# Optimization experiments

Hardware: AMD Instinct MI355X
Metric: run time of the kernel (lower is better)

The kernel has to match this reference:

```python
import jax, jax.numpy as jnp
import numpy as np


def _graph_conv(x, W, b, src, dst, norm_src, norm_dst, n_nodes):
    # DGL GraphConv, norm='both': out = D_in^{-1/2} * A * D_out^{-1/2} * x * W + b
    h = x * norm_src[:, None]                      # [N, d] scale by src out-degree norm
    m = h[src]                                     # [E, d] gather (irregular access)
    agg = jax.ops.segment_sum(m, dst, num_segments=n_nodes)  # [N, d] scatter-add
    agg = agg * norm_dst[:, None]
    return agg @ W + b


def setup_inputs() -> dict:
    key = jax.random.key(0)
    ks = jax.random.split(key, 6)
    N, E, IN, HID = 50000, 800000, 64, 128
    in_feat = jax.random.normal(ks[0], (N, IN), dtype=jnp.float32)
    W1 = jax.random.normal(ks[1], (IN, HID), dtype=jnp.float32) * (1.0 / np.sqrt(IN))
    b1 = jnp.zeros((HID,), dtype=jnp.float32)
    W2 = jax.random.normal(ks[2], (HID, IN), dtype=jnp.float32) * (1.0 / np.sqrt(HID))
    b2 = jnp.zeros((IN,), dtype=jnp.float32)
    src = jax.random.randint(ks[3], (E,), 0, N, dtype=jnp.int32)
    dst = jax.random.randint(ks[4], (E,), 0, N, dtype=jnp.int32)
    return {"in_feat": in_feat, "W1": W1, "b1": b1, "W2": W2, "b2": b2,
            "src": src, "dst": dst, "n_nodes": N}


def reference(in_feat, W1, b1, W2, b2, src, dst, n_nodes):
    ones = jnp.ones(src.shape, dtype=in_feat.dtype)
    deg_out = jax.ops.segment_sum(ones, src, num_segments=n_nodes)
    deg_in = jax.ops.segment_sum(ones, dst, num_segments=n_nodes)
    # DGL clamps degrees to min 1 (allow_zero_in_degree=True just skips the check)
    norm_src = jnp.clip(deg_out, 1.0, None) ** -0.5
    norm_dst = jnp.clip(deg_in, 1.0, None) ** -0.5
    h = _graph_conv(in_feat, W1, b1, src, dst, norm_src, norm_dst, n_nodes)
    h = jax.nn.relu(h)
    h = _graph_conv(h, W2, b2, src, dst, norm_src, norm_dst, n_nodes)
    return h
```

## Files before the change

kernel.cpp:

```cpp
#include <hip/hip_runtime.h>

#define IN_F 64
#define HID_F 128
#define CAP 64
#define CHUNK 4096
#define CAPB 4096
#define MAXB 512

typedef unsigned short u16;
typedef unsigned int u32;
typedef _Float16 f16;
typedef __attribute__((ext_vector_type(4))) _Float16 f16x4;
typedef __attribute__((ext_vector_type(8))) _Float16 f16x8;
typedef __attribute__((ext_vector_type(4))) float f32x4;

__global__ __launch_bounds__(256)
void partition_kernel(const int* __restrict__ src, const int* __restrict__ dst,
                      int* __restrict__ gcurD, int* __restrict__ gcurS,
                      u32* __restrict__ bufD, u16* __restrict__ bufS,
                      int E, int NBUCK) {
    __shared__ int histD[MAXB], histS[MAXB], baseD[MAXB], baseS[MAXB];
    const int t  = threadIdx.x;
    const int e0 = blockIdx.x * CHUNK;
    const int n  = min(CHUNK, E - e0);

    for (int b = t; b < NBUCK; b += 256) { histD[b] = 0; histS[b] = 0; }
    __syncthreads();
    for (int i = t; i < n; i += 256) {
        atomicAdd(&histD[dst[e0 + i] >> 7], 1);
        atomicAdd(&histS[src[e0 + i] >> 7], 1);
    }
    __syncthreads();
    for (int b = t; b < NBUCK; b += 256) {
        baseD[b] = atomicAdd(&gcurD[b], histD[b]);
        baseS[b] = atomicAdd(&gcurS[b], histS[b]);
        histD[b] = 0;
        histS[b] = 0;
    }
    __syncthreads();
    for (int i = t; i < n; i += 256) {
        int d  = dst[e0 + i];
        int s  = src[e0 + i];
        int bD = d >> 7, bS = s >> 7;
        int p  = baseD[bD] + atomicAdd(&histD[bD], 1);
        if (p < CAPB) bufD[(size_t)bD * CAPB + p] = (u32)d | ((u32)s << 16);
        int p2 = baseS[bS] + atomicAdd(&histS[bS], 1);
        if (p2 < CAPB) bufS[(size_t)bS * CAPB + p2] = (u16)s;
    }
}

__global__ __launch_bounds__(256)
void bucket_pass2_kernel(const u32* __restrict__ bufD, const int* __restrict__ gcurD,
                         const u16* __restrict__ bufS, const int* __restrict__ gcurS,
                         u16* __restrict__ slots, int* __restrict__ deg_in,
                         int* __restrict__ deg_out, int N, int NBUCK) {
    __shared__ int lcur[128];
    const int t = threadIdx.x;
    if (t < 128) lcur[t] = 0;
    __syncthreads();
    if (blockIdx.x < NBUCK) {
        const int b = blockIdx.x;
        const int cnt = min(gcurD[b], CAPB);
        const u32* p = bufD + (size_t)b * CAPB;
        for (int i = t; i < cnt; i += 256) {
            u32 v = p[i];
            int d = (int)(v & 0xFFFFu);
            int s = (int)(v >> 16);
            int pos = atomicAdd(&lcur[d & 127], 1);
            if (pos < CAP) slots[(size_t)d * CAP + pos] = (u16)s;
        }
        __syncthreads();
        int node = b * 128 + t;
        if (t < 128 && node < N) deg_in[node] = lcur[t];
    } else {
        const int b = blockIdx.x - NBUCK;
        const int cnt = min(gcurS[b], CAPB);
        const u16* p = bufS + (size_t)b * CAPB;
        for (int i = t; i < cnt; i += 256)
            atomicAdd(&lcur[p[i] & 127], 1);
        __syncthreads();
        int node = b * 128 + t;
        if (t < 128 && node < N) deg_out[node] = lcur[t];
    }
}

__global__ void prep_w_kernel(const float* __restrict__ W1, const float* __restrict__ W2,
                              f16* __restrict__ W1t, f16* __restrict__ W2t) {
    int t = blockIdx.x * blockDim.x + threadIdx.x;
    if (t < IN_F * HID_F) {
        int n = t / IN_F, k = t % IN_F;
        W1t[t] = (f16)W1[k * HID_F + n];
    } else if (t < 2 * IN_F * HID_F) {
        int i = t - IN_F * HID_F;
        int n = i / HID_F, k = i % HID_F;
        W2t[i] = (f16)W2[k * IN_F + n];
    }
}

__global__ void norm_prescale_kernel(const int* __restrict__ dego, const int* __restrict__ degi,
                                     const float* __restrict__ x,
                                     float* __restrict__ norm_src, float* __restrict__ norm_dst,
                                     f16x4* __restrict__ y, int N) {
    int t = blockIdx.x * blockDim.x + threadIdx.x;
    if (t < N * 16) {
        int r = t >> 4;
        int c = t & 15;
        float ns = rsqrtf((float)max(dego[r], 1));
        float4 v = ((const float4*)x)[t];
        f16x4 h;
        h.x = (f16)(v.x * ns); h.y = (f16)(v.y * ns);
        h.z = (f16)(v.z * ns); h.w = (f16)(v.w * ns);
        y[t] = h;
        if (c == 0) {
            norm_src[r] = ns;
            norm_dst[r] = rsqrtf((float)max(degi[r], 1));
        }
    }
}

template <bool DST_EPI>
__global__ void gather_agg_kernel(const f16x4* __restrict__ x, const u16* __restrict__ slots,
                                  const int* __restrict__ deg_in, const float* __restrict__ sd,
                                  const float* __restrict__ bias,
                                  void* __restrict__ outv, int N) {
    int t = blockIdx.x * blockDim.x + threadIdx.x;
    int node = t >> 4;
    int c = t & 15;
    if (node >= N) return;
    int deg = min(deg_in[node], CAP);
    const u16* srow = slots + (size_t)node * CAP;
    float4 acc = make_float4(0.f, 0.f, 0.f, 0.f);

    int i = 0;
    for (; i + 8 <= deg; i += 8) {
        int s[8];
#pragma unroll
        for (int j = 0; j < 8; ++j) s[j] = (int)srow[i + j];
        f16x4 v[8];
#pragma unroll
        for (int j = 0; j < 8; ++j) v[j] = x[(size_t)s[j] * 16 + c];
#pragma unroll
        for (int j = 0; j < 8; ++j) {
            acc.x += (float)v[j].x; acc.y += (float)v[j].y;
            acc.z += (float)v[j].z; acc.w += (float)v[j].w;
        }
    }
    for (; i < deg; ++i) {
        f16x4 v = x[(size_t)srow[i] * 16 + c];
        acc.x += (float)v.x; acc.y += (float)v.y;
        acc.z += (float)v.z; acc.w += (float)v.w;
    }
    if (DST_EPI) {
        float d = sd[node];
        float4 bb = ((const float4*)bias)[c];
        acc.x = acc.x * d + bb.x;
        acc.y = acc.y * d + bb.y;
        acc.z = acc.z * d + bb.z;
        acc.w = acc.w * d + bb.w;
        ((float4*)outv)[t] = acc;
    } else {
        f16x4 h;
        h.x = (f16)acc.x; h.y = (f16)acc.y; h.z = (f16)acc.z; h.w = (f16)acc.w;
        ((f16x4*)outv)[t] = h;
    }
}

template <int K, int NCOL, bool RELU, bool BIAS>
__global__ __launch_bounds__(256)
void gemm_mfma(const f16* __restrict__ A, const f16* __restrict__ Wt,
               const float* __restrict__ bias, const float* __restrict__ rowscale,
               f16* __restrict__ C, int M) {
    constexpr int KT = K / 32;
    constexpr int CT = NCOL / 16;
    const int wave = threadIdx.x >> 6;
    const int lane = threadIdx.x & 63;
    const int nl   = lane & 15;
    const int quad = lane >> 4;
    const int tile = blockIdx.x * 4 + wave;
    if (tile * 16 >= M) return;
    const int r0 = tile * 16;

    f16x8 b[CT][KT];
#pragma unroll
    for (int ct = 0; ct < CT; ++ct)
#pragma unroll
        for (int kf = 0; kf < KT; ++kf)
            b[ct][kf] = *(const f16x8*)(Wt + (ct * 16 + nl) * K + kf * 32 + quad * 8);

    f16x8 a[KT];
#pragma unroll
    for (int kf = 0; kf < KT; ++kf)
        a[kf] = *(const f16x8*)(A + (size_t)(r0 + nl) * K + kf * 32 + quad * 8);

    f32x4 acc[CT];
#pragma unroll
    for (int ct = 0; ct < CT; ++ct) acc[ct] = (f32x4){0.f, 0.f, 0.f, 0.f};
#pragma unroll
    for (int ct = 0; ct < CT; ++ct)
#pragma unroll
        for (int kf = 0; kf < KT; ++kf)
            acc[ct] = __builtin_amdgcn_mfma_f32_16x16x32_f16(a[kf], b[ct][kf], acc[ct], 0, 0, 0);

    float rs[4];
#pragma unroll
    for (int reg = 0; reg < 4; ++reg) rs[reg] = rowscale[r0 + quad * 4 + reg];
#pragma unroll
    for (int ct = 0; ct < CT; ++ct) {
        float bb = BIAS ? bias[ct * 16 + nl] : 0.f;
#pragma unroll
        for (int reg = 0; reg < 4; ++reg) {
            float v = acc[ct][reg] * rs[reg] + bb;
            if (RELU) v = fmaxf(v, 0.f);
            C[(size_t)(r0 + quad * 4 + reg) * NCOL + ct * 16 + nl] = (f16)v;
        }
    }
}

extern "C" void kernel_launch(void* const* d_in, const int* in_sizes, int n_in,
                              void* d_out, int out_size, void* d_ws, size_t ws_size,
                              hipStream_t stream) {
    const float* in_feat = (const float*)d_in[0];
    const float* W1      = (const float*)d_in[1];
    const float* b1      = (const float*)d_in[2];
    const float* W2      = (const float*)d_in[3];
    const float* b2      = (const float*)d_in[4];
    const int*   src     = (const int*)d_in[5];
    const int*   dst     = (const int*)d_in[6];

    const int N = in_sizes[0] / IN_F;
    const int E = in_sizes[5];
    float* out = (float*)d_out;

    const int NBUCK = (N + 127) >> 7;

    int* deg_in  = (int*)d_ws;
    int* deg_out = deg_in + N;
    int* gcurD   = deg_out + N;
    int* gcurS   = gcurD + MAXB;
    u16* slots   = (u16*)(gcurS + MAXB);
    float* norm_src = (float*)(slots + (size_t)N * CAP);
    float* norm_dst = norm_src + N;
    f16* scaled_x = (f16*)(norm_dst + N);
    f16* agg1     = scaled_x + (size_t)N * IN_F;
    f16* h1       = agg1 + (size_t)N * IN_F;
    f16* g2       = h1 + (size_t)N * HID_F;
    f16* W1t      = g2 + (size_t)N * IN_F;
    f16* W2t      = W1t + IN_F * HID_F;
    u32* bufD     = (u32*)(W2t + IN_F * HID_F);
    u16* bufS     = (u16*)(bufD + (size_t)NBUCK * CAPB);

    hipMemsetAsync(gcurD, 0, sizeof(int) * 2 * MAXB, stream);
    prep_w_kernel<<<(2 * IN_F * HID_F + 255) / 256, 256, 0, stream>>>(W1, W2, W1t, W2t);
    partition_kernel<<<(E + CHUNK - 1) / CHUNK, 256, 0, stream>>>(
        src, dst, gcurD, gcurS, bufD, bufS, E, NBUCK);
    bucket_pass2_kernel<<<2 * NBUCK, 256, 0, stream>>>(
        bufD, gcurD, bufS, gcurS, slots, deg_in, deg_out, N, NBUCK);

    const int gthreads = N * 16;
    const int gblocks  = (gthreads + 255) / 256;
    const int mfma_blocks = ((N + 15) / 16 + 3) / 4;

    norm_prescale_kernel<<<gblocks, 256, 0, stream>>>(
        deg_out, deg_in, in_feat, norm_src, norm_dst, (f16x4*)scaled_x, N);

    gather_agg_kernel<false><<<gblocks, 256, 0, stream>>>(
        (const f16x4*)scaled_x, slots, deg_in, nullptr, nullptr, agg1, N);
    gemm_mfma<IN_F, HID_F, true, true><<<mfma_blocks, 256, 0, stream>>>(
        agg1, W1t, b1, norm_dst, h1, N);

    gemm_mfma<HID_F, IN_F, false, false><<<mfma_blocks, 256, 0, stream>>>(
        h1, W2t, nullptr, norm_src, g2, N);
    gather_agg_kernel<true><<<gblocks, 256, 0, stream>>>(
        (const f16x4*)g2, slots, deg_in, norm_dst, b2, out, N);
}
```

Before: 179.8 us.

## Fuse the two MFMA GEMMs through LDS and fold weight prep into partition

The two per-node GEMMs (agg1·W1 with ReLU, then h1·W2 with the source-norm scale) now run in one kernel. The hidden activations stay in per-wave shared memory instead of going through a global h1 buffer, which removes one kernel launch and a write and read of N×128 halves. Weight transposition moves into an extra block of the partition kernel, dropping another launch. The intra-wave handoff through LDS relies on s_waitcnt with no barrier, which assumes wave-synchronous execution, and W fragments are now loaded inside the MFMA loop rather than hoisted.

```diff
diff --git a/kernel.cpp b/kernel.cpp
--- a/kernel.cpp
+++ b/kernel.cpp
@@ -18,7 +18,22 @@
 void partition_kernel(const int* __restrict__ src, const int* __restrict__ dst,
                       int* __restrict__ gcurD, int* __restrict__ gcurS,
                       u32* __restrict__ bufD, u16* __restrict__ bufS,
+                      const float* __restrict__ W1, const float* __restrict__ W2,
+                      f16* __restrict__ W1t, f16* __restrict__ W2t,
                       int E, int NBUCK) {
+    if (blockIdx.x == gridDim.x - 1) {
+        for (int t = threadIdx.x; t < 2 * IN_F * HID_F; t += 256) {
+            if (t < IN_F * HID_F) {
+                int n = t / IN_F, k = t % IN_F;
+                W1t[t] = (f16)W1[k * HID_F + n];
+            } else {
+                int i = t - IN_F * HID_F;
+                int n = i / HID_F, k = i % HID_F;
+                W2t[i] = (f16)W2[k * IN_F + n];
+            }
+        }
+        return;
+    }
     __shared__ int histD[MAXB], histS[MAXB], baseD[MAXB], baseS[MAXB];
     const int t  = threadIdx.x;
     const int e0 = blockIdx.x * CHUNK;
@@ -81,19 +96,6 @@
         __syncthreads();
         int node = b * 128 + t;
         if (t < 128 && node < N) deg_out[node] = lcur[t];
-    }
-}
-
-__global__ void prep_w_kernel(const float* __restrict__ W1, const float* __restrict__ W2,
-                              f16* __restrict__ W1t, f16* __restrict__ W2t) {
-    int t = blockIdx.x * blockDim.x + threadIdx.x;
-    if (t < IN_F * HID_F) {
-        int n = t / IN_F, k = t % IN_F;
-        W1t[t] = (f16)W1[k * HID_F + n];
-    } else if (t < 2 * IN_F * HID_F) {
-        int i = t - IN_F * HID_F;
-        int n = i / HID_F, k = i % HID_F;
-        W2t[i] = (f16)W2[k * IN_F + n];
     }
 }
 
@@ -165,13 +167,13 @@
     }
 }
 
-template <int K, int NCOL, bool RELU, bool BIAS>
 __global__ __launch_bounds__(256)
-void gemm_mfma(const f16* __restrict__ A, const f16* __restrict__ Wt,
-               const float* __restrict__ bias, const float* __restrict__ rowscale,
-               f16* __restrict__ C, int M) {
-    constexpr int KT = K / 32;
-    constexpr int CT = NCOL / 16;
+void gemm_fused(const f16* __restrict__ agg1, const f16* __restrict__ W1t,
+                const float* __restrict__ b1, const float* __restrict__ nd,
+                const float* __restrict__ ns, const f16* __restrict__ W2t,
+                f16* __restrict__ g2, int M) {
+    constexpr int LDH = HID_F + 8;
+    __shared__ f16 h[4][16 * LDH];
     const int wave = threadIdx.x >> 6;
     const int lane = threadIdx.x & 63;
     const int nl   = lane & 15;
@@ -179,41 +181,63 @@
     const int tile = blockIdx.x * 4 + wave;
     if (tile * 16 >= M) return;
     const int r0 = tile * 16;
-
-    f16x8 b[CT][KT];
-#pragma unroll
-    for (int ct = 0; ct < CT; ++ct)
-#pragma unroll
-        for (int kf = 0; kf < KT; ++kf)
-            b[ct][kf] = *(const f16x8*)(Wt + (ct * 16 + nl) * K + kf * 32 + quad * 8);
-
-    f16x8 a[KT];
-#pragma unroll
-    for (int kf = 0; kf < KT; ++kf)
-        a[kf] = *(const f16x8*)(A + (size_t)(r0 + nl) * K + kf * 32 + quad * 8);
-
-    f32x4 acc[CT];
-#pragma unroll
-    for (int ct = 0; ct < CT; ++ct) acc[ct] = (f32x4){0.f, 0.f, 0.f, 0.f};
-#pragma unroll
-    for (int ct = 0; ct < CT; ++ct)
-#pragma unroll
-        for (int kf = 0; kf < KT; ++kf)
-            acc[ct] = __builtin_amdgcn_mfma_f32_16x16x32_f16(a[kf], b[ct][kf], acc[ct], 0, 0, 0);
-
-    float rs[4];
-#pragma unroll
-    for (int reg = 0; reg < 4; ++reg) rs[reg] = rowscale[r0 + quad * 4 + reg];
-#pragma unroll
-    for (int ct = 0; ct < CT; ++ct) {
-        float bb = BIAS ? bias[ct * 16 + nl] : 0.f;
+    f16* hw = h[wave];
+
+    f16x8 a1[2];
+#pragma unroll
+    for (int kf = 0; kf < 2; ++kf)
+        a1[kf] = *(const f16x8*)(agg1 + (size_t)(r0 + nl) * IN_F + kf * 32 + quad * 8);
+
+    f32x4 acc1[8];
+#pragma unroll
+    for (int ct = 0; ct < 8; ++ct) {
+        acc1[ct] = (f32x4){0.f, 0.f, 0.f, 0.f};
+#pragma unroll
+        for (int kf = 0; kf < 2; ++kf) {
+            f16x8 b = *(const f16x8*)(W1t + (ct * 16 + nl) * IN_F + kf * 32 + quad * 8);
+            acc1[ct] = __builtin_amdgcn_mfma_f32_16x16x32_f16(a1[kf], b, acc1[ct], 0, 0, 0);
+        }
+    }
+
+    float rs1[4];
+#pragma unroll
+    for (int reg = 0; reg < 4; ++reg) rs1[reg] = nd[r0 + quad * 4 + reg];
+#pragma unroll
+    for (int ct = 0; ct < 8; ++ct) {
+        float bb = b1[ct * 16 + nl];
 #pragma unroll
         for (int reg = 0; reg < 4; ++reg) {
-            float v = acc[ct][reg] * rs[reg] + bb;
-            if (RELU) v = fmaxf(v, 0.f);
-            C[(size_t)(r0 + quad * 4 + reg) * NCOL + ct * 16 + nl] = (f16)v;
-        }
-    }
+            float v = fmaxf(acc1[ct][reg] * rs1[reg] + bb, 0.f);
+            hw[(quad * 4 + reg) * LDH + ct * 16 + nl] = (f16)v;
+        }
+    }
+    __builtin_amdgcn_s_waitcnt(0);
+
+    f16x8 a2[4];
+#pragma unroll
+    for (int kf = 0; kf < 4; ++kf)
+        a2[kf] = *(const f16x8*)(hw + nl * LDH + kf * 32 + quad * 8);
+
+    f32x4 acc2[4];
+#pragma unroll
+    for (int ct = 0; ct < 4; ++ct) {
+        acc2[ct] = (f32x4){0.f, 0.f, 0.f, 0.f};
+#pragma unroll
+        for (int kf = 0; kf < 4; ++kf) {
+            f16x8 b = *(const f16x8*)(W2t + (ct * 16 + nl) * HID_F + kf * 32 + quad * 8);
+            acc2[ct] = __builtin_amdgcn_mfma_f32_16x16x32_f16(a2[kf], b, acc2[ct], 0, 0, 0);
+        }
+    }
+
+    float rs2[4];
+#pragma unroll
+    for (int reg = 0; reg < 4; ++reg) rs2[reg] = ns[r0 + quad * 4 + reg];
+#pragma unroll
+    for (int ct = 0; ct < 4; ++ct)
+#pragma unroll
+        for (int reg = 0; reg < 4; ++reg)
+            g2[(size_t)(r0 + quad * 4 + reg) * IN_F + ct * 16 + nl] =
+                (f16)(acc2[ct][reg] * rs2[reg]);
 }
 
 extern "C" void kernel_launch(void* const* d_in, const int* in_sizes, int n_in,
@@ -242,34 +266,29 @@
     float* norm_dst = norm_src + N;
     f16* scaled_x = (f16*)(norm_dst + N);
     f16* agg1     = scaled_x + (size_t)N * IN_F;
-    f16* h1       = agg1 + (size_t)N * IN_F;
-    f16* g2       = h1 + (size_t)N * HID_F;
+    f16* g2       = agg1 + (size_t)N * IN_F;
     f16* W1t      = g2 + (size_t)N * IN_F;
     f16* W2t      = W1t + IN_F * HID_F;
     u32* bufD     = (u32*)(W2t + IN_F * HID_F);
     u16* bufS     = (u16*)(bufD + (size_t)NBUCK * CAPB);
 
     hipMemsetAsync(gcurD, 0, sizeof(int) * 2 * MAXB, stream);
-    prep_w_kernel<<<(2 * IN_F * HID_F + 255) / 256, 256, 0, stream>>>(W1, W2, W1t, W2t);
-    partition_kernel<<<(E + CHUNK - 1) / CHUNK, 256, 0, stream>>>(
-        src, dst, gcurD, gcurS, bufD, bufS, E, NBUCK);
+    partition_kernel<<<(E + CHUNK - 1) / CHUNK + 1, 256, 0, stream>>>(
+        src, dst, gcurD, gcurS, bufD, bufS, W1, W2, W1t, W2t, E, NBUCK);
     bucket_pass2_kernel<<<2 * NBUCK, 256, 0, stream>>>(
         bufD, gcurD, bufS, gcurS, slots, deg_in, deg_out, N, NBUCK);
 
     const int gthreads = N * 16;
     const int gblocks  = (gthreads + 255) / 256;
-    const int mfma_blocks = ((N + 15) / 16 + 3) / 4;
 
     norm_prescale_kernel<<<gblocks, 256, 0, stream>>>(
         deg_out, deg_in, in_feat, norm_src, norm_dst, (f16x4*)scaled_x, N);
 
     gather_agg_kernel<false><<<gblocks, 256, 0, stream>>>(
         (const f16x4*)scaled_x, slots, deg_in, nullptr, nullptr, agg1, N);
-    gemm_mfma<IN_F, HID_F, true, true><<<mfma_blocks, 256, 0, stream>>>(
-        agg1, W1t, b1, norm_dst, h1, N);
-
-    gemm_mfma<HID_F, IN_F, false, false><<<mfma_blocks, 256, 0, stream>>>(
-        h1, W2t, nullptr, norm_src, g2, N);
+    gemm_fused<<<((N + 15) / 16 + 3) / 4, 256, 0, stream>>>(
+        agg1, W1t, b1, norm_dst, norm_src, W2t, g2, N);
+
     gather_agg_kernel<true><<<gblocks, 256, 0, stream>>>(
         (const f16x4*)g2, slots, deg_in, norm_dst, b2, out, N);
 }
```

Result: faster. 172.2 us (-4.2%).
